# Kernel tuning notes

Measured on AMD Instinct MI355X. Metric: run time of the kernel, lower is better.

Reference implementation:

```python
import jax, jax.numpy as jnp
import numpy as np
import math

B, N, C = 16, 4096, 256
WS = 8            # window_size
NH = 8            # num_heads
HD = C // NH      # head_dim = 32
LK = 32           # linformer compressed length
G = 16            # global bank tokens


def setup_inputs() -> dict:
    key = jax.random.key(0)
    ks = jax.random.split(key, 10)
    x = jax.random.normal(ks[0], (B, N, C), dtype=jnp.float32)
    W_qkv = jax.random.normal(ks[1], (C, 3 * C), dtype=jnp.float32) * 0.02
    b_qkv = jnp.zeros((3 * C,), dtype=jnp.float32)
    E_k = jax.random.normal(ks[2], (WS * WS, LK), dtype=jnp.float32) * 0.02
    E_v = jax.random.normal(ks[3], (WS * WS, LK), dtype=jnp.float32) * 0.02
    k_bank = jax.random.normal(ks[4], (G, C), dtype=jnp.float32)
    v_bank = jax.random.normal(ks[5], (G, C), dtype=jnp.float32)
    W_proj = jax.random.normal(ks[6], (C, C), dtype=jnp.float32) * 0.02
    b_proj = jnp.zeros((C,), dtype=jnp.float32)
    return {"x": x, "W_qkv": W_qkv, "b_qkv": b_qkv, "E_k": E_k, "E_v": E_v,
            "k_bank": k_bank, "v_bank": v_bank, "W_proj": W_proj, "b_proj": b_proj,
            "window_size": WS, "num_heads": NH}


def reference(x, W_qkv, b_qkv, E_k, E_v, k_bank, v_bank, W_proj, b_proj, window_size, num_heads):
    Bb, Nn, Cc = x.shape
    Hs = int(math.isqrt(Nn))          # H = W = sqrt(N), divisible by window_size here
    ws = window_size
    nh = Hs // ws                      # windows per side
    hd = Cc // num_heads
    NW = ws * ws                       # tokens per window

    # ---- window partition: [B,N,C] -> [BW, NW, C]
    xw = x.reshape(Bb, nh, ws, nh, ws, Cc).transpose(0, 1, 3, 2, 4, 5)
    xw = xw.reshape(Bb * nh * nh, NW, Cc)
    BW = xw.shape[0]

    # ---- qkv projection and head split: (3, BW, H, NW, hd)
    qkv = (xw @ W_qkv + b_qkv).reshape(BW, NW, 3, num_heads, hd)
    qkv = qkv.transpose(2, 0, 3, 1, 4)
    q, k, v = qkv[0], qkv[1], qkv[2]

    # ---- Linformer KV compression: NW == seq_len (no pad branch)
    k_c = jnp.einsum('nk,bhnd->bhkd', E_k, k)   # [BW,H,LK,hd]
    v_c = jnp.einsum('nk,bhnd->bhkd', E_v, v)

    # ---- global memory bank, broadcast to all windows: [BW,H,G,hd]
    Gt = k_bank.shape[0]
    kb = jnp.broadcast_to(k_bank.reshape(Gt, num_heads, hd).transpose(1, 0, 2)[None],
                          (BW, num_heads, Gt, hd))
    vb = jnp.broadcast_to(v_bank.reshape(Gt, num_heads, hd).transpose(1, 0, 2)[None],
                          (BW, num_heads, Gt, hd))

    k_full = jnp.concatenate([k_c, kb], axis=2)  # [BW,H,LK+G,hd]
    v_full = jnp.concatenate([v_c, vb], axis=2)

    # ---- SDPA (dropout_p = 0)
    scale = 1.0 / math.sqrt(hd)
    scores = jnp.einsum('bhqd,bhkd->bhqk', q, k_full) * scale
    attn = jax.nn.softmax(scores, axis=-1)
    out = jnp.einsum('bhqk,bhkd->bhqd', attn, v_full)     # [BW,H,NW,hd]

    out = out.transpose(0, 2, 1, 3).reshape(BW, NW, Cc)
    out = out @ W_proj + b_proj

    # ---- window reverse: [BW,NW,C] -> [B,N,C]
    out = out.reshape(Bb, nh, nh, ws, ws, Cc).transpose(0, 1, 3, 2, 4, 5)
    out = out.reshape(Bb, Hs * Hs, Cc)
    return out
```

## Files before the change

### kernel.cpp

```cpp
#include <hip/hip_runtime.h>


typedef unsigned int uint;
typedef __attribute__((ext_vector_type(8))) short short8;
typedef __attribute__((ext_vector_type(4))) float f32x4;

__device__ __forceinline__ float bup(unsigned short hs) {
    return __uint_as_float(((uint)hs) << 16);
}
__device__ __forceinline__ uint f2b(float f) {
    uint u = __float_as_uint(f);
    return (u + 0x7FFFu + ((u >> 16) & 1u)) >> 16;
}
__device__ __forceinline__ f32x4 mfma16(short8 a, short8 b, f32x4 c) {
    return __builtin_amdgcn_mfma_f32_16x16x32_bf16(a, b, c, 0, 0, 0);
}

#define WS_WHQ 0
#define WS_WHP 196608
#define WS_WLP 262144
#define WS_EKT 327680
#define WS_EVT 329728

__global__ void __launch_bounds__(256)
eswa_prep(const float* __restrict__ Wqkv, const float* __restrict__ Wproj,
          const float* __restrict__ Ek, const float* __restrict__ Ev,
          short* __restrict__ wsp)
{
    const int blk = blockIdx.x, thr = threadIdx.x;
    if (blk < 96) {
        const int g = blk * 256 + thr;
        const int lane = g & 63, tk = (g >> 6) & 7, tn = g >> 9;
        const int quad = lane >> 4, l16 = lane & 15;
        short8 hi;
        #pragma unroll
        for (int j = 0; j < 8; ++j) {
            const int r = tk * 32 + quad * 8 + j;
            const int c = tn * 16 + l16;
            hi[j] = (short)f2b(Wqkv[r * 768 + c]);
        }
        *(short8*)(wsp + WS_WHQ + ((tn * 8 + tk) * 64 + lane) * 8) = hi;
    } else if (blk < 128) {
        const int g = (blk - 96) * 256 + thr;
        const int lane = g & 63, tk = (g >> 6) & 7, tn = g >> 9;
        const int quad = lane >> 4, l16 = lane & 15;
        short8 hi, lo;
        #pragma unroll
        for (int j = 0; j < 8; ++j) {
            const int r = tk * 32 + quad * 8 + j;
            const int c = tn * 16 + l16;
            const float w = Wproj[r * 256 + c];
            const uint h = f2b(w);
            hi[j] = (short)h;
            lo[j] = (short)f2b(w - bup((unsigned short)h));
        }
        const int o = ((tn * 8 + tk) * 64 + lane) * 8;
        *(short8*)(wsp + WS_WHP + o) = hi;
        *(short8*)(wsp + WS_WLP + o) = lo;
    } else {
        const float* E = (blk == 128) ? Ek : Ev;
        const int base = (blk == 128) ? WS_EKT : WS_EVT;
        const int lane = thr & 63, tk = (thr >> 6) & 1, tm = (thr >> 7) & 1;
        const int quad = lane >> 4, l16 = lane & 15;
        short8 v;
        #pragma unroll
        for (int j = 0; j < 8; ++j) {
            const int t = tk * 32 + quad * 8 + j;
            const int lk = tm * 16 + l16;
            v[j] = (short)f2b(E[t * 32 + lk]);
        }
        *(short8*)(wsp + base + ((tm * 2 + tk) * 64 + lane) * 8) = v;
    }
}

#define SMEM_BYTES 148480

__global__ void __launch_bounds__(1024, 4)
eswa_main(const float* __restrict__ x, const float* __restrict__ bqkv,
          const float* __restrict__ kbank, const float* __restrict__ vbank,
          const float* __restrict__ bproj, const short* __restrict__ wsp,
          float* __restrict__ out)
{
    extern __shared__ char smem[];
    short* xh = (short*)smem;

    const int tid  = threadIdx.x;
    const int wave = tid >> 6;
    const int lane = tid & 63;
    const int quad = lane >> 4;
    const int l16  = lane & 15;

    const int b  = blockIdx.x >> 6;
    const int w  = blockIdx.x & 63;
    const int rw = w >> 3;
    const int cw = w & 7;

    #pragma unroll
    for (int i = 0; i < 4; ++i) {
        const int vi = tid + 1024 * i;
        const int t  = vi >> 6;
        const int c  = (vi & 63) * 4;
        const int n  = (rw * 8 + (t >> 3)) * 64 + cw * 8 + (t & 7);
        const float4 xv = *(const float4*)(x + (size_t)(b * 4096 + n) * 256 + c);
        const uint h0 = f2b(xv.x), h1 = f2b(xv.y), h2 = f2b(xv.z), h3 = f2b(xv.w);
        *(uint2*)(xh + t * 264 + c) = make_uint2(h0 | (h1 << 16), h2 | (h3 << 16));
    }
    __syncthreads();

    {
        const short* Whq = wsp + WS_WHQ;
        const int tn0 = wave * 3;
        f32x4 acc[3][4];
        #pragma unroll
        for (int p = 0; p < 3; ++p) {
            const int tn = tn0 + p;
            const int sec = tn >> 4, hh = (tn >> 1) & 7, half = tn & 1;
            const float bv = bqkv[sec * 256 + hh * 32 + half * 16 + l16];
            #pragma unroll
            for (int m = 0; m < 4; ++m) acc[p][m] = (f32x4){bv, bv, bv, bv};
        }
        #pragma unroll 2
        for (int tk = 0; tk < 8; ++tk) {
            short8 af[4];
            #pragma unroll
            for (int m = 0; m < 4; ++m)
                af[m] = *(const short8*)(xh + (m * 16 + l16) * 264 + tk * 32 + quad * 8);
            #pragma unroll
            for (int p = 0; p < 3; ++p) {
                const short8 bh = *(const short8*)(Whq + (((tn0 + p) * 8 + tk) * 64 + lane) * 8);
                #pragma unroll
                for (int m = 0; m < 4; ++m)
                    acc[p][m] = mfma16(af[m], bh, acc[p][m]);
            }
        }
        #pragma unroll
        for (int p = 0; p < 3; ++p) {
            const int tn = tn0 + p;
            const int sec = tn >> 4, hh = (tn >> 1) & 7, half = tn & 1;
            short* arena = (short*)(smem + 33792 + hh * 14336);
            #pragma unroll
            for (int m = 0; m < 4; ++m) {
                #pragma unroll
                for (int r = 0; r < 4; ++r) {
                    const int t = m * 16 + quad * 4 + r;
                    const float v = acc[p][m][r];
                    if (sec == 0)
                        arena[t * 40 + half * 16 + l16] =
                            (short)f2b(v * 0.17677669529663687f);
                    else if (sec == 1)
                        (arena + 2560)[(half * 16 + l16) * 72 + t] = (short)f2b(v);
                    else
                        (arena + 4864)[(half * 16 + l16) * 72 + t] = (short)f2b(v);
                }
            }
        }
    }
    __syncthreads();

    const int h = wave >> 1, s = wave & 1;
    short* arena = (short*)(smem + 33792 + h * 14336);
    short* qsb = arena;
    short* kTb = arena + 2560;
    short* vTb = arena + 4864;
    const int gB  = s * 8 + (lane >> 3);
    const int dqB = (lane & 7) * 4;

    short8 kB[2][2], vB[2][2];
    #pragma unroll
    for (int tn = 0; tn < 2; ++tn)
        #pragma unroll
        for (int tk = 0; tk < 2; ++tk) {
            kB[tn][tk] = *(const short8*)(kTb + (tn * 16 + l16) * 72 + tk * 32 + quad * 8);
            vB[tn][tk] = *(const short8*)(vTb + (tn * 16 + l16) * 72 + tk * 32 + quad * 8);
        }
    short8 akE[2], avE[2];
    #pragma unroll
    for (int tk = 0; tk < 2; ++tk) {
        akE[tk] = *(const short8*)(wsp + WS_EKT + ((s * 2 + tk) * 64 + lane) * 8);
        avE[tk] = *(const short8*)(wsp + WS_EVT + ((s * 2 + tk) * 64 + lane) * 8);
    }
    const float4 kbv = *(const float4*)(kbank + gB * 256 + h * 32 + dqB);
    const float4 vbv = *(const float4*)(vbank + gB * 256 + h * 32 + dqB);
    __syncthreads();

    {
        f32x4 kc[2], vc[2];
        #pragma unroll
        for (int tn = 0; tn < 2; ++tn) { kc[tn] = (f32x4){0,0,0,0}; vc[tn] = (f32x4){0,0,0,0}; }
        #pragma unroll
        for (int tk = 0; tk < 2; ++tk)
            #pragma unroll
            for (int tn = 0; tn < 2; ++tn) {
                kc[tn] = mfma16(akE[tk], kB[tn][tk], kc[tn]);
                vc[tn] = mfma16(avE[tk], vB[tn][tk], vc[tn]);
            }
        #pragma unroll
        for (int tn = 0; tn < 2; ++tn)
            #pragma unroll
            for (int r = 0; r < 4; ++r) {
                const int lk = s * 16 + quad * 4 + r;
                const int d  = tn * 16 + l16;
                kTb[lk * 40 + d] = (short)f2b(kc[tn][r]);
                vTb[d * 72 + lk] = (short)f2b(vc[tn][r]);
            }
        kTb[(32 + gB) * 40 + dqB + 0] = (short)f2b(kbv.x);
        kTb[(32 + gB) * 40 + dqB + 1] = (short)f2b(kbv.y);
        kTb[(32 + gB) * 40 + dqB + 2] = (short)f2b(kbv.z);
        kTb[(32 + gB) * 40 + dqB + 3] = (short)f2b(kbv.w);
        vTb[(dqB + 0) * 72 + 32 + gB] = (short)f2b(vbv.x);
        vTb[(dqB + 1) * 72 + 32 + gB] = (short)f2b(vbv.y);
        vTb[(dqB + 2) * 72 + 32 + gB] = (short)f2b(vbv.z);
        vTb[(dqB + 3) * 72 + 32 + gB] = (short)f2b(vbv.w);
        if (s == 0)
            *(uint4*)(vTb + (lane >> 1) * 72 + 48 + (lane & 1) * 8) = make_uint4(0, 0, 0, 0);
    }
    __syncthreads();

    f32x4 sc[2][3];
    f32x4 inv4[2];
    {
        short8 qA[2], kfB[3];
        #pragma unroll
        for (int ml = 0; ml < 2; ++ml)
            qA[ml] = *(const short8*)(qsb + ((2 * s + ml) * 16 + l16) * 40 + quad * 8);
        #pragma unroll
        for (int n = 0; n < 3; ++n)
            kfB[n] = *(const short8*)(kTb + (n * 16 + l16) * 40 + quad * 8);
        #pragma unroll
        for (int ml = 0; ml < 2; ++ml)
            #pragma unroll
            for (int n = 0; n < 3; ++n) {
                sc[ml][n] = (f32x4){0, 0, 0, 0};
                sc[ml][n] = mfma16(qA[ml], kfB[n], sc[ml][n]);
            }
        #pragma unroll
        for (int ml = 0; ml < 2; ++ml) {
            #pragma unroll
            for (int r = 0; r < 4; ++r) {
                float mm = fmaxf(fmaxf(sc[ml][0][r], sc[ml][1][r]), sc[ml][2][r]);
                mm = fmaxf(mm, __shfl_xor(mm, 1));
                mm = fmaxf(mm, __shfl_xor(mm, 2));
                mm = fmaxf(mm, __shfl_xor(mm, 4));
                mm = fmaxf(mm, __shfl_xor(mm, 8));
                const float e0 = __expf(sc[ml][0][r] - mm);
                const float e1 = __expf(sc[ml][1][r] - mm);
                const float e2 = __expf(sc[ml][2][r] - mm);
                sc[ml][0][r] = e0; sc[ml][1][r] = e1; sc[ml][2][r] = e2;
                float su = e0 + e1 + e2;
                su += __shfl_xor(su, 1);
                su += __shfl_xor(su, 2);
                su += __shfl_xor(su, 4);
                su += __shfl_xor(su, 8);
                inv4[ml][r] = 1.0f / su;
            }
        }
    }
    __syncthreads();

    {
        short* Pb = (s == 0) ? qsb : kTb;
        #pragma unroll
        for (int ml = 0; ml < 2; ++ml)
            #pragma unroll
            for (int n = 0; n < 3; ++n)
                #pragma unroll
                for (int r = 0; r < 4; ++r)
                    Pb[(ml * 16 + quad * 4 + r) * 72 + n * 16 + l16] =
                        (short)f2b(sc[ml][n][r] * inv4[ml][r]);
        *(uint4*)(Pb + (lane >> 1) * 72 + 48 + (lane & 1) * 8) = make_uint4(0, 0, 0, 0);

        short8 vfB[2][2], pA[2][2];
        #pragma unroll
        for (int tn = 0; tn < 2; ++tn)
            #pragma unroll
            for (int tk = 0; tk < 2; ++tk)
                vfB[tn][tk] = *(const short8*)(vTb + (tn * 16 + l16) * 72 + tk * 32 + quad * 8);
        #pragma unroll
        for (int ml = 0; ml < 2; ++ml)
            #pragma unroll
            for (int tk = 0; tk < 2; ++tk)
                pA[ml][tk] = *(const short8*)(Pb + (ml * 16 + l16) * 72 + tk * 32 + quad * 8);
        #pragma unroll
        for (int ml = 0; ml < 2; ++ml)
            #pragma unroll
            for (int tn = 0; tn < 2; ++tn) {
                f32x4 oa = (f32x4){0, 0, 0, 0};
                oa = mfma16(pA[ml][0], vfB[tn][0], oa);
                oa = mfma16(pA[ml][1], vfB[tn][1], oa);
                #pragma unroll
                for (int r = 0; r < 4; ++r) {
                    const int t = s * 32 + ml * 16 + quad * 4 + r;
                    ((short*)smem)[h * 2048 + t * 32 + tn * 16 + l16] =
                        (short)f2b(oa[r]);
                }
            }
    }
    __syncthreads();

    {
        const short* Whp = wsp + WS_WHP;
        const short* Wlp = wsp + WS_WLP;
        const short* attnS = (const short*)smem;
        const int tn = wave;
        f32x4 acc[4];
        {
            const float bi = bproj[tn * 16 + l16];
            #pragma unroll
            for (int m = 0; m < 4; ++m) acc[m] = (f32x4){bi, bi, bi, bi};
        }
        #pragma unroll 2
        for (int tk = 0; tk < 8; ++tk) {
            short8 aA[4];
            #pragma unroll
            for (int m = 0; m < 4; ++m)
                aA[m] = *(const short8*)(attnS + tk * 2048 + (m * 16 + l16) * 32 + quad * 8);
            const int bo = ((tn * 8 + tk) * 64 + lane) * 8;
            const short8 bh = *(const short8*)(Whp + bo);
            const short8 bl = *(const short8*)(Wlp + bo);
            #pragma unroll
            for (int m = 0; m < 4; ++m) {
                acc[m] = mfma16(aA[m], bh, acc[m]);
                acc[m] = mfma16(aA[m], bl, acc[m]);
            }
        }
        #pragma unroll
        for (int m = 0; m < 4; ++m)
            #pragma unroll
            for (int r = 0; r < 4; ++r) {
                const int t = m * 16 + quad * 4 + r;
                const int n = (rw * 8 + (t >> 3)) * 64 + cw * 8 + (t & 7);
                out[(size_t)(b * 4096 + n) * 256 + tn * 16 + l16] = acc[m][r];
            }
    }
}

extern "C" void kernel_launch(void* const* d_in, const int* in_sizes, int n_in,
                              void* d_out, int out_size, void* d_ws, size_t ws_size,
                              hipStream_t stream) {
    const float* x     = (const float*)d_in[0];
    const float* Wqkv  = (const float*)d_in[1];
    const float* bqkv  = (const float*)d_in[2];
    const float* Ek    = (const float*)d_in[3];
    const float* Ev    = (const float*)d_in[4];
    const float* kbank = (const float*)d_in[5];
    const float* vbank = (const float*)d_in[6];
    const float* Wproj = (const float*)d_in[7];
    const float* bproj = (const float*)d_in[8];
    float* outp        = (float*)d_out;
    short* wsp         = (short*)d_ws;
    (void)in_sizes; (void)n_in; (void)out_size; (void)ws_size;

    hipFuncSetAttribute((const void*)eswa_main,
                        hipFuncAttributeMaxDynamicSharedMemorySize, SMEM_BYTES);

    eswa_prep<<<130, 256, 0, stream>>>(Wqkv, Wproj, Ek, Ev, wsp);
    eswa_main<<<1024, 1024, SMEM_BYTES, stream>>>(x, bqkv, kbank, vbank, bproj,
                                                  wsp, outp);
}
```

Measured before the change: 208.1 us.

## Replace padded LDS layouts with XOR swizzles and use packed bf16 conversion

All shared-memory tiles (x tile, q/k/v arenas, P buffer, attention output) switch from padded row strides to unpadded rows with XOR-swizzled column indices. This shrinks the LDS footprint from 148480 to 131072 bytes while still avoiding bank conflicts. Float-to-bf16 rounding now uses the HIP packed intrinsic for pairs of values, and the prep kernel splits its work across twice as many blocks. Swizzle patterns must match on every write and read, otherwise results silently break.

```diff
diff --git a/kernel.cpp b/kernel.cpp
--- a/kernel.cpp
+++ b/kernel.cpp
@@ -1,20 +1,32 @@
 #include <hip/hip_runtime.h>
+#include <hip/hip_bf16.h>
 
 
 typedef unsigned int uint;
 typedef __attribute__((ext_vector_type(8))) short short8;
 typedef __attribute__((ext_vector_type(4))) float f32x4;
 
-__device__ __forceinline__ float bup(unsigned short hs) {
-    return __uint_as_float(((uint)hs) << 16);
+__device__ __forceinline__ float bup(uint hs) {
+    return __uint_as_float(hs << 16);
 }
 __device__ __forceinline__ uint f2b(float f) {
-    uint u = __float_as_uint(f);
-    return (u + 0x7FFFu + ((u >> 16) & 1u)) >> 16;
+    __hip_bfloat16 h = __float2bfloat16(f);
+    unsigned short u;
+    __builtin_memcpy(&u, &h, 2);
+    return (uint)u;
+}
+__device__ __forceinline__ uint f2b2(float a, float b) {
+    __hip_bfloat162 h = __float22bfloat162_rn(make_float2(a, b));
+    uint u;
+    __builtin_memcpy(&u, &h, 4);
+    return u;
 }
 __device__ __forceinline__ f32x4 mfma16(short8 a, short8 b, f32x4 c) {
     return __builtin_amdgcn_mfma_f32_16x16x32_bf16(a, b, c, 0, 0, 0);
 }
+__device__ __forceinline__ int sw256(int r, int c) { return r * 256 + (c ^ ((r & 7) << 3)); }
+__device__ __forceinline__ int sw64 (int r, int c) { return r * 64  + (c ^ ((r & 7) << 3)); }
+__device__ __forceinline__ int sw32 (int r, int c) { return r * 32  + (c ^ ((r & 3) << 3)); }
 
 #define WS_WHQ 0
 #define WS_WHP 196608
@@ -28,52 +40,51 @@
           short* __restrict__ wsp)
 {
     const int blk = blockIdx.x, thr = threadIdx.x;
-    if (blk < 96) {
-        const int g = blk * 256 + thr;
+    if (blk < 192) {
+        const int jh = blk & 1;
+        const int g = (blk >> 1) * 256 + thr;
         const int lane = g & 63, tk = (g >> 6) & 7, tn = g >> 9;
         const int quad = lane >> 4, l16 = lane & 15;
-        short8 hi;
-        #pragma unroll
-        for (int j = 0; j < 8; ++j) {
-            const int r = tk * 32 + quad * 8 + j;
-            const int c = tn * 16 + l16;
-            hi[j] = (short)f2b(Wqkv[r * 768 + c]);
-        }
-        *(short8*)(wsp + WS_WHQ + ((tn * 8 + tk) * 64 + lane) * 8) = hi;
-    } else if (blk < 128) {
-        const int g = (blk - 96) * 256 + thr;
+        const int c = tn * 16 + l16;
+        const int r0 = tk * 32 + quad * 8 + jh * 4;
+        const float w0 = Wqkv[(r0 + 0) * 768 + c], w1 = Wqkv[(r0 + 1) * 768 + c];
+        const float w2 = Wqkv[(r0 + 2) * 768 + c], w3 = Wqkv[(r0 + 3) * 768 + c];
+        *(uint2*)(wsp + WS_WHQ + ((tn * 8 + tk) * 64 + lane) * 8 + jh * 4) =
+            make_uint2(f2b2(w0, w1), f2b2(w2, w3));
+    } else if (blk < 256) {
+        const int idx = blk - 192, jh = idx & 1;
+        const int g = (idx >> 1) * 256 + thr;
         const int lane = g & 63, tk = (g >> 6) & 7, tn = g >> 9;
         const int quad = lane >> 4, l16 = lane & 15;
-        short8 hi, lo;
-        #pragma unroll
-        for (int j = 0; j < 8; ++j) {
-            const int r = tk * 32 + quad * 8 + j;
-            const int c = tn * 16 + l16;
-            const float w = Wproj[r * 256 + c];
-            const uint h = f2b(w);
-            hi[j] = (short)h;
-            lo[j] = (short)f2b(w - bup((unsigned short)h));
-        }
-        const int o = ((tn * 8 + tk) * 64 + lane) * 8;
-        *(short8*)(wsp + WS_WHP + o) = hi;
-        *(short8*)(wsp + WS_WLP + o) = lo;
+        const int c = tn * 16 + l16;
+        const int r0 = tk * 32 + quad * 8 + jh * 4;
+        float w[4];
+        #pragma unroll
+        for (int j = 0; j < 4; ++j) w[j] = Wproj[(r0 + j) * 256 + c];
+        const uint h01 = f2b2(w[0], w[1]), h23 = f2b2(w[2], w[3]);
+        const float l0 = w[0] - bup(h01 & 0xffffu), l1 = w[1] - bup(h01 >> 16);
+        const float l2 = w[2] - bup(h23 & 0xffffu), l3 = w[3] - bup(h23 >> 16);
+        const int o = ((tn * 8 + tk) * 64 + lane) * 8 + jh * 4;
+        *(uint2*)(wsp + WS_WHP + o) = make_uint2(h01, h23);
+        *(uint2*)(wsp + WS_WLP + o) = make_uint2(f2b2(l0, l1), f2b2(l2, l3));
     } else {
-        const float* E = (blk == 128) ? Ek : Ev;
-        const int base = (blk == 128) ? WS_EKT : WS_EVT;
+        const float* E = (blk == 256) ? Ek : Ev;
+        const int base = (blk == 256) ? WS_EKT : WS_EVT;
         const int lane = thr & 63, tk = (thr >> 6) & 1, tm = (thr >> 7) & 1;
         const int quad = lane >> 4, l16 = lane & 15;
-        short8 v;
-        #pragma unroll
-        for (int j = 0; j < 8; ++j) {
-            const int t = tk * 32 + quad * 8 + j;
-            const int lk = tm * 16 + l16;
-            v[j] = (short)f2b(E[t * 32 + lk]);
-        }
-        *(short8*)(wsp + base + ((tm * 2 + tk) * 64 + lane) * 8) = v;
-    }
-}
-
-#define SMEM_BYTES 148480
+        const int lk = tm * 16 + l16;
+        uint pk[4];
+        #pragma unroll
+        for (int jp = 0; jp < 4; ++jp) {
+            const int t = tk * 32 + quad * 8 + jp * 2;
+            pk[jp] = f2b2(E[t * 32 + lk], E[(t + 1) * 32 + lk]);
+        }
+        *(uint4*)(wsp + base + ((tm * 2 + tk) * 64 + lane) * 8) =
+            make_uint4(pk[0], pk[1], pk[2], pk[3]);
+    }
+}
+
+#define SMEM_BYTES 131072
 
 __global__ void __launch_bounds__(1024, 4)
 eswa_main(const float* __restrict__ x, const float* __restrict__ bqkv,
@@ -102,8 +113,7 @@
         const int c  = (vi & 63) * 4;
         const int n  = (rw * 8 + (t >> 3)) * 64 + cw * 8 + (t & 7);
         const float4 xv = *(const float4*)(x + (size_t)(b * 4096 + n) * 256 + c);
-        const uint h0 = f2b(xv.x), h1 = f2b(xv.y), h2 = f2b(xv.z), h3 = f2b(xv.w);
-        *(uint2*)(xh + t * 264 + c) = make_uint2(h0 | (h1 << 16), h2 | (h3 << 16));
+        *(uint2*)(xh + sw256(t, c)) = make_uint2(f2b2(xv.x, xv.y), f2b2(xv.z, xv.w));
     }
     __syncthreads();
 
@@ -124,7 +134,7 @@
             short8 af[4];
             #pragma unroll
             for (int m = 0; m < 4; ++m)
-                af[m] = *(const short8*)(xh + (m * 16 + l16) * 264 + tk * 32 + quad * 8);
+                af[m] = *(const short8*)(xh + sw256(m * 16 + l16, tk * 32 + quad * 8));
             #pragma unroll
             for (int p = 0; p < 3; ++p) {
                 const short8 bh = *(const short8*)(Whq + (((tn0 + p) * 8 + tk) * 64 + lane) * 8);
@@ -137,7 +147,7 @@
         for (int p = 0; p < 3; ++p) {
             const int tn = tn0 + p;
             const int sec = tn >> 4, hh = (tn >> 1) & 7, half = tn & 1;
-            short* arena = (short*)(smem + 33792 + hh * 14336);
+            short* arena = (short*)(smem + 32768 + hh * 12288);
             #pragma unroll
             for (int m = 0; m < 4; ++m) {
                 #pragma unroll
@@ -145,12 +155,12 @@
                     const int t = m * 16 + quad * 4 + r;
                     const float v = acc[p][m][r];
                     if (sec == 0)
-                        arena[t * 40 + half * 16 + l16] =
+                        arena[sw32(t, half * 16 + l16)] =
                             (short)f2b(v * 0.17677669529663687f);
                     else if (sec == 1)
-                        (arena + 2560)[(half * 16 + l16) * 72 + t] = (short)f2b(v);
+                        (arena + 2048)[sw64(half * 16 + l16, t)] = (short)f2b(v);
                     else
-                        (arena + 4864)[(half * 16 + l16) * 72 + t] = (short)f2b(v);
+                        (arena + 4096)[sw64(half * 16 + l16, t)] = (short)f2b(v);
                 }
             }
         }
@@ -158,10 +168,10 @@
     __syncthreads();
 
     const int h = wave >> 1, s = wave & 1;
-    short* arena = (short*)(smem + 33792 + h * 14336);
-    short* qsb = arena;
-    short* kTb = arena + 2560;
-    short* vTb = arena + 4864;
+    short* arena = (short*)(smem + 32768 + h * 12288);
+    short* qsp = arena;
+    short* kTp = arena + 2048;
+    short* vTp = arena + 4096;
     const int gB  = s * 8 + (lane >> 3);
     const int dqB = (lane & 7) * 4;
 
@@ -170,8 +180,8 @@
     for (int tn = 0; tn < 2; ++tn)
         #pragma unroll
         for (int tk = 0; tk < 2; ++tk) {
-            kB[tn][tk] = *(const short8*)(kTb + (tn * 16 + l16) * 72 + tk * 32 + quad * 8);
-            vB[tn][tk] = *(const short8*)(vTb + (tn * 16 + l16) * 72 + tk * 32 + quad * 8);
+            kB[tn][tk] = *(const short8*)(kTp + sw64(tn * 16 + l16, tk * 32 + quad * 8));
+            vB[tn][tk] = *(const short8*)(vTp + sw64(tn * 16 + l16, tk * 32 + quad * 8));
         }
     short8 akE[2], avE[2];
     #pragma unroll
@@ -200,19 +210,17 @@
             for (int r = 0; r < 4; ++r) {
                 const int lk = s * 16 + quad * 4 + r;
                 const int d  = tn * 16 + l16;
-                kTb[lk * 40 + d] = (short)f2b(kc[tn][r]);
-                vTb[d * 72 + lk] = (short)f2b(vc[tn][r]);
-            }
-        kTb[(32 + gB) * 40 + dqB + 0] = (short)f2b(kbv.x);
-        kTb[(32 + gB) * 40 + dqB + 1] = (short)f2b(kbv.y);
-        kTb[(32 + gB) * 40 + dqB + 2] = (short)f2b(kbv.z);
-        kTb[(32 + gB) * 40 + dqB + 3] = (short)f2b(kbv.w);
-        vTb[(dqB + 0) * 72 + 32 + gB] = (short)f2b(vbv.x);
-        vTb[(dqB + 1) * 72 + 32 + gB] = (short)f2b(vbv.y);
-        vTb[(dqB + 2) * 72 + 32 + gB] = (short)f2b(vbv.z);
-        vTb[(dqB + 3) * 72 + 32 + gB] = (short)f2b(vbv.w);
+                kTp[sw32(lk, d)] = (short)f2b(kc[tn][r]);
+                vTp[sw64(d, lk)] = (short)f2b(vc[tn][r]);
+            }
+        *(uint2*)(kTp + sw32(32 + gB, dqB)) =
+            make_uint2(f2b2(kbv.x, kbv.y), f2b2(kbv.z, kbv.w));
+        vTp[sw64(dqB + 0, 32 + gB)] = (short)f2b(vbv.x);
+        vTp[sw64(dqB + 1, 32 + gB)] = (short)f2b(vbv.y);
+        vTp[sw64(dqB + 2, 32 + gB)] = (short)f2b(vbv.z);
+        vTp[sw64(dqB + 3, 32 + gB)] = (short)f2b(vbv.w);
         if (s == 0)
-            *(uint4*)(vTb + (lane >> 1) * 72 + 48 + (lane & 1) * 8) = make_uint4(0, 0, 0, 0);
+            *(uint4*)(vTp + sw64(lane >> 1, 48 + (lane & 1) * 8)) = make_uint4(0, 0, 0, 0);
     }
     __syncthreads();
 
@@ -222,10 +230,10 @@
         short8 qA[2], kfB[3];
         #pragma unroll
         for (int ml = 0; ml < 2; ++ml)
-            qA[ml] = *(const short8*)(qsb + ((2 * s + ml) * 16 + l16) * 40 + quad * 8);
+            qA[ml] = *(const short8*)(qsp + sw32((2 * s + ml) * 16 + l16, quad * 8));
         #pragma unroll
         for (int n = 0; n < 3; ++n)
-            kfB[n] = *(const short8*)(kTb + (n * 16 + l16) * 40 + quad * 8);
+            kfB[n] = *(const short8*)(kTp + sw32(n * 16 + l16, quad * 8));
         #pragma unroll
         for (int ml = 0; ml < 2; ++ml)
             #pragma unroll
@@ -258,28 +266,28 @@
     __syncthreads();
 
     {
-        short* Pb = (s == 0) ? qsb : kTb;
+        short* Pb = (s == 0) ? qsp : kTp;
         #pragma unroll
         for (int ml = 0; ml < 2; ++ml)
             #pragma unroll
             for (int n = 0; n < 3; ++n)
                 #pragma unroll
                 for (int r = 0; r < 4; ++r)
-                    Pb[(ml * 16 + quad * 4 + r) * 72 + n * 16 + l16] =
+                    Pb[sw64(ml * 16 + quad * 4 + r, n * 16 + l16)] =
                         (short)f2b(sc[ml][n][r] * inv4[ml][r]);
-        *(uint4*)(Pb + (lane >> 1) * 72 + 48 + (lane & 1) * 8) = make_uint4(0, 0, 0, 0);
+        *(uint4*)(Pb + sw64(lane >> 1, 48 + (lane & 1) * 8)) = make_uint4(0, 0, 0, 0);
 
         short8 vfB[2][2], pA[2][2];
         #pragma unroll
         for (int tn = 0; tn < 2; ++tn)
             #pragma unroll
             for (int tk = 0; tk < 2; ++tk)
-                vfB[tn][tk] = *(const short8*)(vTb + (tn * 16 + l16) * 72 + tk * 32 + quad * 8);
+                vfB[tn][tk] = *(const short8*)(vTp + sw64(tn * 16 + l16, tk * 32 + quad * 8));
         #pragma unroll
         for (int ml = 0; ml < 2; ++ml)
             #pragma unroll
             for (int tk = 0; tk < 2; ++tk)
-                pA[ml][tk] = *(const short8*)(Pb + (ml * 16 + l16) * 72 + tk * 32 + quad * 8);
+                pA[ml][tk] = *(const short8*)(Pb + sw64(ml * 16 + l16, tk * 32 + quad * 8));
         #pragma unroll
         for (int ml = 0; ml < 2; ++ml)
             #pragma unroll
@@ -290,7 +298,7 @@
                 #pragma unroll
                 for (int r = 0; r < 4; ++r) {
                     const int t = s * 32 + ml * 16 + quad * 4 + r;
-                    ((short*)smem)[h * 2048 + t * 32 + tn * 16 + l16] =
+                    ((short*)smem)[sw256(t, h * 32 + tn * 16 + l16)] =
                         (short)f2b(oa[r]);
                 }
             }
@@ -313,7 +321,7 @@
             short8 aA[4];
             #pragma unroll
             for (int m = 0; m < 4; ++m)
-                aA[m] = *(const short8*)(attnS + tk * 2048 + (m * 16 + l16) * 32 + quad * 8);
+                aA[m] = *(const short8*)(attnS + sw256(m * 16 + l16, tk * 32 + quad * 8));
             const int bo = ((tn * 8 + tk) * 64 + lane) * 8;
             const short8 bh = *(const short8*)(Whp + bo);
             const short8 bl = *(const short8*)(Wlp + bo);
@@ -353,7 +361,7 @@
     hipFuncSetAttribute((const void*)eswa_main,
                         hipFuncAttributeMaxDynamicSharedMemorySize, SMEM_BYTES);
 
-    eswa_prep<<<130, 256, 0, stream>>>(Wqkv, Wproj, Ek, Ev, wsp);
+    eswa_prep<<<258, 256, 0, stream>>>(Wqkv, Wproj, Ek, Ev, wsp);
     eswa_main<<<1024, 1024, SMEM_BYTES, stream>>>(x, bqkv, kbank, vbank, bproj,
                                                   wsp, outp);
 }
```

Result: no change. 208.7 us (+0.3%).
